# Kernel tuning notes

Hardware: AMD Instinct MI355X
Metric: run time of the kernel (lower is better)

The kernel has to match this reference:

```python
import jax, jax.numpy as jnp
import numpy as np
from functools import partial

N_NODES = 50000
N_EDGES = 600000
N_FEAT = 128
HID = [128, 64, 32, 16]
N_GRAPHS = 64
N_CLASSES = 10


def gcn_conv(x, W, b, src, dst, n_nodes):
    # PyG GCNConv: h = x @ W; propagate with symmetric norm over A + I; add bias.
    h = x @ W  # [N, out]
    ones = jnp.ones((src.shape[0],), dtype=x.dtype)
    deg = jax.ops.segment_sum(ones, dst, num_segments=n_nodes) + 1.0  # self-loop
    dinv = jax.lax.rsqrt(deg)
    coef = dinv[src] * dinv[dst]  # [E]
    agg = jax.ops.segment_sum(h[src] * coef[:, None], dst, num_segments=n_nodes)
    agg = agg + h * (dinv * dinv)[:, None]  # self-loop contribution
    return agg + b


def global_mean_pool(x, batch, n_graphs):
    s = jax.ops.segment_sum(x, batch, num_segments=n_graphs)
    cnt = jax.ops.segment_sum(jnp.ones((x.shape[0],), x.dtype), batch, num_segments=n_graphs)
    return s / jnp.maximum(cnt, 1.0)[:, None]


def setup_inputs() -> dict:
    key = jax.random.key(0)
    ks = jax.random.split(key, 16)
    x = jax.random.normal(ks[0], (N_NODES, N_FEAT), dtype=jnp.float32)
    edge_index = jax.random.randint(ks[1], (2, N_EDGES), 0, N_NODES, dtype=jnp.int64)
    batch = jnp.sort(jax.random.randint(ks[2], (N_NODES,), 0, N_GRAPHS, dtype=jnp.int64))

    def glorot(k, fan_in, fan_out):
        s = float(np.sqrt(6.0 / (fan_in + fan_out)))
        return jax.random.uniform(k, (fan_in, fan_out), jnp.float32, -s, s)

    dims = [N_FEAT] + HID
    params = {}
    for i in range(4):
        params[f"W{i+1}"] = glorot(ks[3 + i], dims[i], dims[i + 1])
        params[f"b{i+1}"] = jnp.zeros((dims[i + 1],), jnp.float32)
    params["Wlin"] = glorot(ks[7], HID[-1], N_CLASSES)
    params["blin"] = jnp.zeros((N_CLASSES,), jnp.float32)
    return {"x": x, "edge_index": edge_index, "batch": batch, **params}


def reference(x, edge_index, batch, W1, b1, W2, b2, W3, b3, W4, b4, Wlin, blin):
    src, dst = edge_index[0], edge_index[1]
    n = x.shape[0]
    h = jax.nn.relu(gcn_conv(x, W1, b1, src, dst, n))
    h = jax.nn.relu(gcn_conv(h, W2, b2, src, dst, n))
    h = jax.nn.relu(gcn_conv(h, W3, b3, src, dst, n))
    h = jax.nn.relu(gcn_conv(h, W4, b4, src, dst, n))
    g = global_mean_pool(h, batch, N_GRAPHS)  # [G, 16]
    return g @ Wlin + blin
```

## Files before the change

### kernel.cpp

```cpp
#include <hip/hip_runtime.h>
#include <hip/hip_bf16.h>


#define N_GRAPHS 64
#define N_CLASSES 10

typedef short bf8_t __attribute__((ext_vector_type(8)));
typedef float f4_t  __attribute__((ext_vector_type(4)));

__device__ __forceinline__ float b2f(unsigned int u) {
  return __uint_as_float(u << 16);
}
__device__ __forceinline__ unsigned short f2b(float f) {
  unsigned int x = __float_as_uint(f);
  x += 0x7fffu + ((x >> 16) & 1u);
  return (unsigned short)(x >> 16);
}

__device__ __forceinline__ void block_detect(const unsigned int* __restrict__ xraw,
    const unsigned int* __restrict__ eraw, int* f32, int* i64) {
  __shared__ int c_bf, c_nz;
  if (threadIdx.x == 0) { c_bf = 0; c_nz = 0; }
  __syncthreads();
  unsigned int d = xraw[threadIdx.x & 255];
  int e = (int)(((d & 0xffffu) >> 7) & 0xff);
  if (e >= 100 && e <= 140) atomicAdd(&c_bf, 1);
  if (eraw && threadIdx.x < 64 && eraw[2 * threadIdx.x + 1] != 0u) atomicAdd(&c_nz, 1);
  __syncthreads();
  *f32 = (c_bf < 150) ? 1 : 0;
  if (i64) *i64 = (c_nz == 0) ? 1 : 0;
}

struct WPtrs { const void* p[10]; };
static constexpr int WSEG[10] = {16384, 128, 8192, 64, 2048, 32, 512, 16, 160, 10};
static constexpr int WTOTAL   = 27546;
static constexpr int WOFF[10] = {0, 16384, 16512, 24704, 24768, 26816, 26848, 27360, 27376, 27536};

__global__ __launch_bounds__(256) void cvt_we_kernel(
    const unsigned int* __restrict__ xraw, WPtrs wp, unsigned short* __restrict__ wc,
    const int* __restrict__ braw, int* __restrict__ b32,
    const int* __restrict__ eraw, int* __restrict__ deg,
    int BW, int BB, int n, int E) {
  int f32, i64;
  block_detect(xraw, (const unsigned int*)eraw, &f32, &i64);
  const int bid = blockIdx.x;
  if (bid < BW) {
    int i = bid * 256 + threadIdx.x;
    if (i >= WTOTAL) return;
    int off = i, s = 0;
    #pragma unroll
    for (int t = 0; t < 10; ++t) {
      if (s == 0 && off >= WSEG[t]) { off -= WSEG[t]; } else if (s == 0) { s = t + 1; }
    }
    s -= 1;
    int soff = off;
    if ((s & 1) == 0 && s <= 6) {
      int KB, FOUT;
      if (s == 0)      { KB = 4; FOUT = 128; }
      else if (s == 2) { KB = 4; FOUT = 64; }
      else if (s == 4) { KB = 2; FOUT = 32; }
      else             { KB = 1; FOUT = 16; }
      int j = off & 7, l = (off >> 3) & 63, f = off >> 9;
      int ct = f / KB, kb = f - ct * KB;
      int k = kb * 32 + ((l >> 4) << 3) + j;
      int nn = ct * 16 + (l & 15);
      soff = k * FOUT + nn;
    }
    const void* p = wp.p[s];
    wc[WOFF[s] + off] = f32 ? f2b(((const float*)p)[soff])
                            : ((const unsigned short*)p)[soff];
  } else if (bid < BW + BB) {
    int i = (bid - BW) * 256 + threadIdx.x;
    if (i < n) b32[i] = i64 ? braw[2 * i] : braw[i];
  } else {
    int e = (bid - BW - BB) * 256 + threadIdx.x;
    if (e >= E) return;
    int d = i64 ? eraw[2 * (E + e)] : eraw[E + e];
    atomicAdd(&deg[d], 1);
  }
}

__global__ __launch_bounds__(256) void scan_kernel(const int* __restrict__ deg,
    int* __restrict__ row_ptr, int* __restrict__ cursor, float* __restrict__ dinv,
    unsigned long long* __restrict__ desc, int n) {
  __shared__ int ws[4];
  __shared__ int s_total;
  __shared__ unsigned int s_prev;
  const int b = blockIdx.x, tid = threadIdx.x, lane = tid & 63, wv = tid >> 6;
  const int i = b * 256 + tid;
  int v = (i < n) ? deg[i] : 0;
  int x = v;
  #pragma unroll
  for (int off = 1; off < 64; off <<= 1) {
    int y = __shfl_up(x, off, 64);
    if (lane >= off) x += y;
  }
  if (lane == 63) ws[wv] = x;
  __syncthreads();
  int wbase = 0;
  for (int w = 0; w < wv; ++w) wbase += ws[w];
  int incl = x + wbase;
  if (tid == 0) {
    int tot = ws[0] + ws[1] + ws[2] + ws[3];
    s_total = tot;
    unsigned long long st = (b == 0) ? (2ULL << 62) : (1ULL << 62);
    atomicExch(&desc[b], st | (unsigned long long)(unsigned int)tot);
    if (b == 0) s_prev = 0u;
  }
  __syncthreads();
  if (b > 0 && wv == 0) {
    unsigned int running = 0;
    int j = b - 1;
    while (true) {
      int idx = j - lane;
      unsigned long long d;
      if (idx >= 0) {
        do { d = atomicAdd(&desc[idx], 0ULL); } while ((d >> 62) == 0ULL);
      } else {
        d = (2ULL << 62);
      }
      unsigned long long ball = __ballot((d >> 62) == 2ULL);
      int fp = ball ? (__ffsll((unsigned long long)ball) - 1) : 64;
      unsigned int contrib = (lane <= fp) ? (unsigned int)(d & 0xffffffffULL) : 0u;
      #pragma unroll
      for (int o = 32; o; o >>= 1) contrib += __shfl_xor(contrib, o, 64);
      running += contrib;
      if (fp < 64) break;
      j -= 64;
    }
    if (lane == 0) {
      atomicExch(&desc[b], (2ULL << 62) |
                 (unsigned long long)(unsigned int)(running + (unsigned int)s_total));
      s_prev = running;
    }
  }
  __syncthreads();
  int tot = (int)s_prev + incl;
  if (i < n) {
    row_ptr[i + 1] = tot;
    cursor[i] = tot - v;
    dinv[i] = rsqrtf((float)v + 1.0f);
  }
  if (i == 0) row_ptr[0] = 0;
}

__global__ __launch_bounds__(256) void fill_gemm1_kernel(
    const int* __restrict__ eraw, const unsigned int* __restrict__ xraw,
    int* __restrict__ cursor, const float* __restrict__ dinv,
    uint2* __restrict__ csr,
    const unsigned short* __restrict__ Wf, unsigned short* __restrict__ H,
    int BE, int n, int E) {
  int f32, i64;
  block_detect(xraw, (const unsigned int*)eraw, &f32, &i64);
  if (blockIdx.x < BE) {
    int e = blockIdx.x * 256 + threadIdx.x;
    if (e < E) {
      int s, d;
      if (i64) { s = eraw[2 * e]; d = eraw[2 * (E + e)]; }
      else     { s = eraw[e];     d = eraw[E + e]; }
      int pos = atomicAdd(&cursor[d], 1);
      uint2 v;
      v.x = (unsigned int)s;
      v.y = __float_as_uint(dinv[s] * dinv[d]);
      csr[pos] = v;
    }
    return;
  }
  const int b2 = blockIdx.x - BE;
  const int l = threadIdx.x & 63;
  const int r16 = l & 15, quad = l >> 4;
  const int m0 = (b2 * 4 + (threadIdx.x >> 6)) * 32;
  if (m0 >= n) return;
  bf8_t afrag[2][4];
  #pragma unroll
  for (int mt = 0; mt < 2; ++mt) {
    int node = m0 + mt * 16 + r16;
    int nc = node < n ? node : n - 1;
    if (f32) {
      const float* xp = (const float*)xraw + (size_t)nc * 128 + quad * 8;
      #pragma unroll
      for (int kb = 0; kb < 4; ++kb) {
        const float4* p4 = (const float4*)(xp + kb * 32);
        float4 u0 = p4[0], u1 = p4[1];
        bf8_t a;
        a[0] = (short)f2b(u0.x); a[1] = (short)f2b(u0.y);
        a[2] = (short)f2b(u0.z); a[3] = (short)f2b(u0.w);
        a[4] = (short)f2b(u1.x); a[5] = (short)f2b(u1.y);
        a[6] = (short)f2b(u1.z); a[7] = (short)f2b(u1.w);
        afrag[mt][kb] = a;
      }
    } else {
      const unsigned short* xp = (const unsigned short*)xraw + (size_t)nc * 128 + quad * 8;
      #pragma unroll
      for (int kb = 0; kb < 4; ++kb)
        afrag[mt][kb] = *(const bf8_t*)(xp + kb * 32);
    }
  }
  #pragma unroll
  for (int ct = 0; ct < 8; ++ct) {
    bf8_t bfrag[4];
    #pragma unroll
    for (int kb = 0; kb < 4; ++kb)
      bfrag[kb] = *(const bf8_t*)(Wf + ((ct * 4 + kb) * 64 + l) * 8);
    #pragma unroll
    for (int mt = 0; mt < 2; ++mt) {
      f4_t acc = {0.f, 0.f, 0.f, 0.f};
      #pragma unroll
      for (int kb = 0; kb < 4; ++kb)
        acc = __builtin_amdgcn_mfma_f32_16x16x32_bf16(afrag[mt][kb], bfrag[kb], acc, 0, 0, 0);
      #pragma unroll
      for (int r = 0; r < 4; ++r) {
        int node = m0 + mt * 16 + quad * 4 + r;
        if (node < n)
          H[(size_t)node * 128 + ct * 16 + r16] = f2b(acc[r]);
      }
    }
  }
}

template<int DW> struct UVec { unsigned int d[DW]; };
template<int DW>
__device__ __forceinline__ UVec<DW> uload(const unsigned int* p) {
  UVec<DW> r;
  if constexpr (DW == 4) { uint4 v = *(const uint4*)p; r.d[0]=v.x; r.d[1]=v.y; r.d[2]=v.z; r.d[3]=v.w; }
  else if constexpr (DW == 2) { uint2 v = *(const uint2*)p; r.d[0]=v.x; r.d[1]=v.y; }
  else { r.d[0] = *p; }
  return r;
}
template<int DW>
__device__ __forceinline__ void ustore(unsigned int* p, const UVec<DW>& v) {
  if constexpr (DW == 4) { *(uint4*)p = make_uint4(v.d[0], v.d[1], v.d[2], v.d[3]); }
  else if constexpr (DW == 2) { *(uint2*)p = make_uint2(v.d[0], v.d[1]); }
  else { *p = v.d[0]; }
}

template<int FIN, int FOUT, int LPG>
__global__ __launch_bounds__(256) void aggemm_kernel(
    const unsigned short* __restrict__ Hin,
    const int* __restrict__ row_ptr, const uint2* __restrict__ csr,
    const float* __restrict__ dinv, const unsigned short* __restrict__ bias,
    const unsigned short* __restrict__ Wf, unsigned short* __restrict__ Hout, int n) {
  constexpr int DW  = FIN / LPG / 2;
  constexpr int NPB = 256 / LPG;
  constexpr int LD  = FIN + 8;
  constexpr int KB  = FIN / 32;
  constexpr int CT  = FOUT / 16;
  constexpr int MT  = NPB / 16;
  __shared__ unsigned short T[NPB * LD];
  const int r = threadIdx.x / LPG, l = threadIdx.x % LPG;
  const int node0 = blockIdx.x * NPB;
  const int g = node0 + r;
  const unsigned int* H2 = (const unsigned int*)Hin;
  UVec<DW> o;
  #pragma unroll
  for (int d = 0; d < DW; ++d) o.d[d] = 0u;
  if (g < n) {
    float di = dinv[g];
    float c0 = di * di;
    float a[2 * DW];
    UVec<DW> hv = uload<DW>(H2 + (size_t)g * (FIN / 2) + l * DW);
    #pragma unroll
    for (int d = 0; d < DW; ++d) {
      a[2*d]   = b2f(hv.d[d] & 0xffffu) * c0;
      a[2*d+1] = b2f(hv.d[d] >> 16) * c0;
    }
    const int e0 = row_ptr[g], e1 = row_ptr[g + 1];
    for (int base = e0; base < e1; base += LPG) {
      int cnt = e1 - base < LPG ? e1 - base : LPG;
      uint2 my = csr[(base + l < e1) ? (base + l) : (e1 - 1)];
      for (int j = 0; j < cnt; ++j) {
        int s = __shfl((int)my.x, j, LPG);
        float c = __uint_as_float(__shfl((int)my.y, j, LPG));
        UVec<DW> v = uload<DW>(H2 + (size_t)s * (FIN / 2) + l * DW);
        #pragma unroll
        for (int d = 0; d < DW; ++d) {
          a[2*d]   = fmaf(b2f(v.d[d] & 0xffffu), c, a[2*d]);
          a[2*d+1] = fmaf(b2f(v.d[d] >> 16), c, a[2*d+1]);
        }
      }
    }
    UVec<DW> bb = uload<DW>((const unsigned int*)bias + l * DW);
    #pragma unroll
    for (int d = 0; d < DW; ++d) {
      float lo = fmaxf(a[2*d]   + b2f(bb.d[d] & 0xffffu), 0.f);
      float hi = fmaxf(a[2*d+1] + b2f(bb.d[d] >> 16), 0.f);
      o.d[d] = (unsigned int)f2b(lo) | ((unsigned int)f2b(hi) << 16);
    }
  }
  ustore<DW>((unsigned int*)&T[r * LD + l * DW * 2], o);
  __syncthreads();
  const int w = threadIdx.x >> 6;
  if (w < MT * CT && node0 < n) {
    const int mt = w / CT, ct = w % CT;
    const int ll = threadIdx.x & 63;
    const int r16 = ll & 15, quad = ll >> 4;
    bf8_t afrag[KB], bfrag[KB];
    #pragma unroll
    for (int kb = 0; kb < KB; ++kb) {
      afrag[kb] = *(const bf8_t*)(&T[(mt * 16 + r16) * LD + quad * 8 + kb * 32]);
      bfrag[kb] = *(const bf8_t*)(Wf + ((ct * KB + kb) * 64 + ll) * 8);
    }
    f4_t acc = {0.f, 0.f, 0.f, 0.f};
    #pragma unroll
    for (int kb = 0; kb < KB; ++kb)
      acc = __builtin_amdgcn_mfma_f32_16x16x32_bf16(afrag[kb], bfrag[kb], acc, 0, 0, 0);
    #pragma unroll
    for (int rr = 0; rr < 4; ++rr) {
      int node = node0 + mt * 16 + quad * 4 + rr;
      if (node < n)
        Hout[(size_t)node * FOUT + ct * 16 + r16] = f2b(acc[rr]);
    }
  }
}

__global__ __launch_bounds__(256) void agg_pool_kernel(
    const unsigned short* __restrict__ Hin,
    const int* __restrict__ row_ptr, const uint2* __restrict__ csr,
    const float* __restrict__ dinv, const unsigned short* __restrict__ bias,
    const int* __restrict__ batch, float* __restrict__ pooled,
    float* __restrict__ cnt, int n) {
  __shared__ float acc[N_GRAPHS * 16];
  __shared__ float ccnt[N_GRAPHS];
  for (int i = threadIdx.x; i < N_GRAPHS * 16; i += 256) acc[i] = 0.f;
  if (threadIdx.x < N_GRAPHS) ccnt[threadIdx.x] = 0.f;
  __syncthreads();
  const int r = threadIdx.x >> 3, l = threadIdx.x & 7;
  const int g = blockIdx.x * 32 + r;
  if (g < n) {
    const unsigned int* H2 = (const unsigned int*)Hin;
    float di = dinv[g];
    float c0 = di * di;
    unsigned int hv = H2[(size_t)g * 8 + l];
    float a0 = b2f(hv & 0xffffu) * c0;
    float a1 = b2f(hv >> 16) * c0;
    const int e0 = row_ptr[g], e1 = row_ptr[g + 1];
    for (int base = e0; base < e1; base += 8) {
      int cnt2 = e1 - base < 8 ? e1 - base : 8;
      uint2 my = csr[(base + l < e1) ? (base + l) : (e1 - 1)];
      for (int j = 0; j < cnt2; ++j) {
        int s = __shfl((int)my.x, j, 8);
        float c = __uint_as_float(__shfl((int)my.y, j, 8));
        unsigned int v = H2[(size_t)s * 8 + l];
        a0 = fmaf(b2f(v & 0xffffu), c, a0);
        a1 = fmaf(b2f(v >> 16), c, a1);
      }
    }
    unsigned int bb = ((const unsigned int*)bias)[l];
    a0 = fmaxf(a0 + b2f(bb & 0xffffu), 0.f);
    a1 = fmaxf(a1 + b2f(bb >> 16), 0.f);
    int gb = batch[g];
    atomicAdd(&acc[gb * 16 + l * 2 + 0], a0);
    atomicAdd(&acc[gb * 16 + l * 2 + 1], a1);
    if (l == 0) atomicAdd(&ccnt[gb], 1.f);
  }
  __syncthreads();
  for (int i = threadIdx.x; i < N_GRAPHS * 16; i += 256)
    if (acc[i] != 0.f) atomicAdd(&pooled[i], acc[i]);
  if (threadIdx.x < N_GRAPHS && ccnt[threadIdx.x] != 0.f)
    atomicAdd(&cnt[threadIdx.x], ccnt[threadIdx.x]);
}

__global__ __launch_bounds__(256) void final_kernel(const float* __restrict__ pooled,
    const float* __restrict__ cnt, const unsigned short* __restrict__ wc,
    void* __restrict__ out, const unsigned int* __restrict__ xraw) {
  int f32;
  block_detect(xraw, nullptr, &f32, nullptr);
  int id = blockIdx.x * 256 + threadIdx.x;
  if (id >= N_GRAPHS * N_CLASSES) return;
  const unsigned short* Wlin = wc + WOFF[8];
  const unsigned short* blin = wc + WOFF[9];
  int g = id / N_CLASSES, c = id - g * N_CLASSES;
  float inv = 1.0f / fmaxf(cnt[g], 1.0f);
  float a = b2f(blin[c]);
  #pragma unroll
  for (int f = 0; f < 16; ++f)
    a = fmaf(pooled[g * 16 + f] * inv, b2f(Wlin[f * N_CLASSES + c]), a);
  if (f32) ((float*)out)[id] = a;
  else     ((unsigned short*)out)[id] = f2b(a);
}

extern "C" void kernel_launch(void* const* d_in, const int* in_sizes, int n_in,
                              void* d_out, int out_size, void* d_ws, size_t ws_size,
                              hipStream_t stream) {
  const unsigned int* xraw = (const unsigned int*)d_in[0];
  const int* eraw          = (const int*)d_in[1];
  const int* braw          = (const int*)d_in[2];

  const int N = in_sizes[2];
  const int E = in_sizes[1] / 2;
  const int nb = (N + 255) / 256;

  char* p = (char*)d_ws;
  auto alloc = [&](size_t bytes) -> void* {
    void* r = (void*)p;
    p += (bytes + 255) & ~(size_t)255;
    return r;
  };
  const size_t off_desc = ((size_t)N * 4 + 255) & ~(size_t)255;
  const size_t off_pool = (off_desc + (size_t)nb * 8 + 255) & ~(size_t)255;
  const size_t ztotal   = off_pool + (N_GRAPHS * 16 + N_GRAPHS) * 4;
  char* zbase = (char*)alloc(ztotal);
  int*   deg    = (int*)zbase;
  unsigned long long* desc = (unsigned long long*)(zbase + off_desc);
  float* pooled = (float*)(zbase + off_pool);
  float* cntf   = pooled + N_GRAPHS * 16;

  int*   row_ptr  = (int*)  alloc((size_t)(N + 1) * 4);
  int*   cursor   = (int*)  alloc((size_t)N * 4);
  float* dinv     = (float*)alloc((size_t)N * 4);
  int*   batch32  = (int*)  alloc((size_t)N * 4);
  uint2* csr      = (uint2*)alloc((size_t)E * 8);
  unsigned short* wcan  = (unsigned short*)alloc((size_t)WTOTAL * 2);
  unsigned short* hbufA = (unsigned short*)alloc((size_t)N * 128 * 2);
  unsigned short* hbufB = (unsigned short*)alloc((size_t)N * 128 * 2);

  hipMemsetAsync(zbase, 0, ztotal, stream);

  WPtrs wp;
  for (int i = 0; i < 10; ++i) wp.p[i] = d_in[3 + i];

  const int BW = (WTOTAL + 255) / 256;
  const int BB = nb;
  const int BE = (E + 255) / 256;
  cvt_we_kernel<<<BW + BB + BE, 256, 0, stream>>>(xraw, wp, wcan, braw, batch32,
      eraw, deg, BW, BB, N, E);

  scan_kernel<<<nb, 256, 0, stream>>>(deg, row_ptr, cursor, dinv, desc, N);

  const unsigned short* W1 = wcan + WOFF[0];
  const unsigned short* b1 = wcan + WOFF[1];
  const unsigned short* W2 = wcan + WOFF[2];
  const unsigned short* b2 = wcan + WOFF[3];
  const unsigned short* W3 = wcan + WOFF[4];
  const unsigned short* b3 = wcan + WOFF[5];
  const unsigned short* W4 = wcan + WOFF[6];
  const unsigned short* b4 = wcan + WOFF[7];

  const int G1 = (N + 127) / 128;
  fill_gemm1_kernel<<<BE + G1, 256, 0, stream>>>(eraw, xraw, cursor, dinv, csr,
      W1, hbufA, BE, N, E);

  aggemm_kernel<128, 64, 16><<<(N + 15) / 16, 256, 0, stream>>>(
      hbufA, row_ptr, csr, dinv, b1, W2, hbufB, N);
  aggemm_kernel<64, 32, 8><<<(N + 31) / 32, 256, 0, stream>>>(
      hbufB, row_ptr, csr, dinv, b2, W3, hbufA, N);
  aggemm_kernel<32, 16, 8><<<(N + 31) / 32, 256, 0, stream>>>(
      hbufA, row_ptr, csr, dinv, b3, W4, hbufB, N);
  agg_pool_kernel<<<(N + 31) / 32, 256, 0, stream>>>(hbufB, row_ptr, csr, dinv, b4,
      batch32, pooled, cntf, N);

  final_kernel<<<(N_GRAPHS * N_CLASSES + 255) / 256, 256, 0, stream>>>(pooled, cntf, wcan, d_out, xraw);
}
```

Before: 240.2 us.

## Fold symmetric norm into GEMM outputs and shard degree/cursor atomics eightfold

Each GEMM now scales its output rows by dinv[src], and each aggregation scales the summed neighbour rows by dinv[dst] at the end. This removes the per-edge coefficient, so the CSR holds only 4-byte source indices instead of 8-byte pairs and the inner loop is a plain add. Separately, the degree counts and fill cursors are split into 8 sub-arrays chosen by block index to cut atomic contention. The scan runs over 8N entries, and its shuffle reduction rebuilds the full degree. The cost is a larger scan and an extra bf16 rounding of the pre-scaled features.

```diff
diff --git a/kernel.cpp b/kernel.cpp
--- a/kernel.cpp
+++ b/kernel.cpp
@@ -39,7 +39,7 @@
 __global__ __launch_bounds__(256) void cvt_we_kernel(
     const unsigned int* __restrict__ xraw, WPtrs wp, unsigned short* __restrict__ wc,
     const int* __restrict__ braw, int* __restrict__ b32,
-    const int* __restrict__ eraw, int* __restrict__ deg,
+    const int* __restrict__ eraw, int* __restrict__ degs,
     int BW, int BB, int n, int E) {
   int f32, i64;
   block_detect(xraw, (const unsigned int*)eraw, &f32, &i64);
@@ -76,11 +76,11 @@
     int e = (bid - BW - BB) * 256 + threadIdx.x;
     if (e >= E) return;
     int d = i64 ? eraw[2 * (E + e)] : eraw[E + e];
-    atomicAdd(&deg[d], 1);
-  }
-}
-
-__global__ __launch_bounds__(256) void scan_kernel(const int* __restrict__ deg,
+    atomicAdd(&degs[(bid & 7) * n + d], 1);
+  }
+}
+
+__global__ __launch_bounds__(256) void scan_kernel(const int* __restrict__ degs,
     int* __restrict__ row_ptr, int* __restrict__ cursor, float* __restrict__ dinv,
     unsigned long long* __restrict__ desc, int n) {
   __shared__ int ws[4];
@@ -88,7 +88,8 @@
   __shared__ unsigned int s_prev;
   const int b = blockIdx.x, tid = threadIdx.x, lane = tid & 63, wv = tid >> 6;
   const int i = b * 256 + tid;
-  int v = (i < n) ? deg[i] : 0;
+  const int d = i >> 3, s = i & 7;
+  int v = (d < n) ? degs[s * n + d] : 0;
   int x = v;
   #pragma unroll
   for (int off = 1; off < 64; off <<= 1) {
@@ -113,15 +114,15 @@
     int j = b - 1;
     while (true) {
       int idx = j - lane;
-      unsigned long long d;
+      unsigned long long dsc;
       if (idx >= 0) {
-        do { d = atomicAdd(&desc[idx], 0ULL); } while ((d >> 62) == 0ULL);
+        do { dsc = atomicAdd(&desc[idx], 0ULL); } while ((dsc >> 62) == 0ULL);
       } else {
-        d = (2ULL << 62);
+        dsc = (2ULL << 62);
       }
-      unsigned long long ball = __ballot((d >> 62) == 2ULL);
+      unsigned long long ball = __ballot((dsc >> 62) == 2ULL);
       int fp = ball ? (__ffsll((unsigned long long)ball) - 1) : 64;
-      unsigned int contrib = (lane <= fp) ? (unsigned int)(d & 0xffffffffULL) : 0u;
+      unsigned int contrib = (lane <= fp) ? (unsigned int)(dsc & 0xffffffffULL) : 0u;
       #pragma unroll
       for (int o = 32; o; o >>= 1) contrib += __shfl_xor(contrib, o, 64);
       running += contrib;
@@ -136,10 +137,16 @@
   }
   __syncthreads();
   int tot = (int)s_prev + incl;
-  if (i < n) {
-    row_ptr[i + 1] = tot;
-    cursor[i] = tot - v;
-    dinv[i] = rsqrtf((float)v + 1.0f);
+  int rs = v;
+  rs += __shfl_xor(rs, 1, 64);
+  rs += __shfl_xor(rs, 2, 64);
+  rs += __shfl_xor(rs, 4, 64);
+  if (d < n) {
+    cursor[s * n + d] = tot - v;
+    if (s == 7) {
+      row_ptr[d + 1] = tot;
+      dinv[d] = rsqrtf((float)rs + 1.0f);
+    }
   }
   if (i == 0) row_ptr[0] = 0;
 }
@@ -147,7 +154,7 @@
 __global__ __launch_bounds__(256) void fill_gemm1_kernel(
     const int* __restrict__ eraw, const unsigned int* __restrict__ xraw,
     int* __restrict__ cursor, const float* __restrict__ dinv,
-    uint2* __restrict__ csr,
+    int* __restrict__ csr_src,
     const unsigned short* __restrict__ Wf, unsigned short* __restrict__ H,
     int BE, int n, int E) {
   int f32, i64;
@@ -158,11 +165,8 @@
       int s, d;
       if (i64) { s = eraw[2 * e]; d = eraw[2 * (E + e)]; }
       else     { s = eraw[e];     d = eraw[E + e]; }
-      int pos = atomicAdd(&cursor[d], 1);
-      uint2 v;
-      v.x = (unsigned int)s;
-      v.y = __float_as_uint(dinv[s] * dinv[d]);
-      csr[pos] = v;
+      int pos = atomicAdd(&cursor[(blockIdx.x & 7) * n + d], 1);
+      csr_src[pos] = s;
     }
     return;
   }
@@ -172,10 +176,16 @@
   const int m0 = (b2 * 4 + (threadIdx.x >> 6)) * 32;
   if (m0 >= n) return;
   bf8_t afrag[2][4];
+  float dv[2][4];
   #pragma unroll
   for (int mt = 0; mt < 2; ++mt) {
     int node = m0 + mt * 16 + r16;
     int nc = node < n ? node : n - 1;
+    #pragma unroll
+    for (int r = 0; r < 4; ++r) {
+      int nd = m0 + mt * 16 + quad * 4 + r;
+      dv[mt][r] = dinv[nd < n ? nd : n - 1];
+    }
     if (f32) {
       const float* xp = (const float*)xraw + (size_t)nc * 128 + quad * 8;
       #pragma unroll
@@ -212,7 +222,7 @@
       for (int r = 0; r < 4; ++r) {
         int node = m0 + mt * 16 + quad * 4 + r;
         if (node < n)
-          H[(size_t)node * 128 + ct * 16 + r16] = f2b(acc[r]);
+          H[(size_t)node * 128 + ct * 16 + r16] = f2b(acc[r] * dv[mt][r]);
       }
     }
   }
@@ -237,7 +247,7 @@
 template<int FIN, int FOUT, int LPG>
 __global__ __launch_bounds__(256) void aggemm_kernel(
     const unsigned short* __restrict__ Hin,
-    const int* __restrict__ row_ptr, const uint2* __restrict__ csr,
+    const int* __restrict__ row_ptr, const int* __restrict__ csr_src,
     const float* __restrict__ dinv, const unsigned short* __restrict__ bias,
     const unsigned short* __restrict__ Wf, unsigned short* __restrict__ Hout, int n) {
   constexpr int DW  = FIN / LPG / 2;
@@ -255,35 +265,33 @@
   #pragma unroll
   for (int d = 0; d < DW; ++d) o.d[d] = 0u;
   if (g < n) {
-    float di = dinv[g];
-    float c0 = di * di;
     float a[2 * DW];
     UVec<DW> hv = uload<DW>(H2 + (size_t)g * (FIN / 2) + l * DW);
     #pragma unroll
     for (int d = 0; d < DW; ++d) {
-      a[2*d]   = b2f(hv.d[d] & 0xffffu) * c0;
-      a[2*d+1] = b2f(hv.d[d] >> 16) * c0;
+      a[2*d]   = b2f(hv.d[d] & 0xffffu);
+      a[2*d+1] = b2f(hv.d[d] >> 16);
     }
     const int e0 = row_ptr[g], e1 = row_ptr[g + 1];
     for (int base = e0; base < e1; base += LPG) {
       int cnt = e1 - base < LPG ? e1 - base : LPG;
-      uint2 my = csr[(base + l < e1) ? (base + l) : (e1 - 1)];
+      int my = csr_src[(base + l < e1) ? (base + l) : (e1 - 1)];
       for (int j = 0; j < cnt; ++j) {
-        int s = __shfl((int)my.x, j, LPG);
-        float c = __uint_as_float(__shfl((int)my.y, j, LPG));
+        int s = __shfl(my, j, LPG);
         UVec<DW> v = uload<DW>(H2 + (size_t)s * (FIN / 2) + l * DW);
         #pragma unroll
         for (int d = 0; d < DW; ++d) {
-          a[2*d]   = fmaf(b2f(v.d[d] & 0xffffu), c, a[2*d]);
-          a[2*d+1] = fmaf(b2f(v.d[d] >> 16), c, a[2*d+1]);
+          a[2*d]   += b2f(v.d[d] & 0xffffu);
+          a[2*d+1] += b2f(v.d[d] >> 16);
         }
       }
     }
+    float di = dinv[g];
     UVec<DW> bb = uload<DW>((const unsigned int*)bias + l * DW);
     #pragma unroll
     for (int d = 0; d < DW; ++d) {
-      float lo = fmaxf(a[2*d]   + b2f(bb.d[d] & 0xffffu), 0.f);
-      float hi = fmaxf(a[2*d+1] + b2f(bb.d[d] >> 16), 0.f);
+      float lo = fmaxf(fmaf(a[2*d],   di, b2f(bb.d[d] & 0xffffu)), 0.f);
+      float hi = fmaxf(fmaf(a[2*d+1], di, b2f(bb.d[d] >> 16)), 0.f);
       o.d[d] = (unsigned int)f2b(lo) | ((unsigned int)f2b(hi) << 16);
     }
   }
@@ -294,6 +302,12 @@
     const int mt = w / CT, ct = w % CT;
     const int ll = threadIdx.x & 63;
     const int r16 = ll & 15, quad = ll >> 4;
+    float dvv[4];
+    #pragma unroll
+    for (int rr = 0; rr < 4; ++rr) {
+      int nd = node0 + mt * 16 + quad * 4 + rr;
+      dvv[rr] = dinv[nd < n ? nd : n - 1];
+    }
     bf8_t afrag[KB], bfrag[KB];
     #pragma unroll
     for (int kb = 0; kb < KB; ++kb) {
@@ -308,14 +322,14 @@
     for (int rr = 0; rr < 4; ++rr) {
       int node = node0 + mt * 16 + quad * 4 + rr;
       if (node < n)
-        Hout[(size_t)node * FOUT + ct * 16 + r16] = f2b(acc[rr]);
+        Hout[(size_t)node * FOUT + ct * 16 + r16] = f2b(acc[rr] * dvv[rr]);
     }
   }
 }
 
 __global__ __launch_bounds__(256) void agg_pool_kernel(
     const unsigned short* __restrict__ Hin,
-    const int* __restrict__ row_ptr, const uint2* __restrict__ csr,
+    const int* __restrict__ row_ptr, const int* __restrict__ csr_src,
     const float* __restrict__ dinv, const unsigned short* __restrict__ bias,
     const int* __restrict__ batch, float* __restrict__ pooled,
     float* __restrict__ cnt, int n) {
@@ -328,26 +342,24 @@
   const int g = blockIdx.x * 32 + r;
   if (g < n) {
     const unsigned int* H2 = (const unsigned int*)Hin;
-    float di = dinv[g];
-    float c0 = di * di;
     unsigned int hv = H2[(size_t)g * 8 + l];
-    float a0 = b2f(hv & 0xffffu) * c0;
-    float a1 = b2f(hv >> 16) * c0;
+    float a0 = b2f(hv & 0xffffu);
+    float a1 = b2f(hv >> 16);
     const int e0 = row_ptr[g], e1 = row_ptr[g + 1];
     for (int base = e0; base < e1; base += 8) {
       int cnt2 = e1 - base < 8 ? e1 - base : 8;
-      uint2 my = csr[(base + l < e1) ? (base + l) : (e1 - 1)];
+      int my = csr_src[(base + l < e1) ? (base + l) : (e1 - 1)];
       for (int j = 0; j < cnt2; ++j) {
-        int s = __shfl((int)my.x, j, 8);
-        float c = __uint_as_float(__shfl((int)my.y, j, 8));
+        int s = __shfl(my, j, 8);
         unsigned int v = H2[(size_t)s * 8 + l];
-        a0 = fmaf(b2f(v & 0xffffu), c, a0);
-        a1 = fmaf(b2f(v >> 16), c, a1);
+        a0 += b2f(v & 0xffffu);
+        a1 += b2f(v >> 16);
       }
     }
+    float di = dinv[g];
     unsigned int bb = ((const unsigned int*)bias)[l];
-    a0 = fmaxf(a0 + b2f(bb & 0xffffu), 0.f);
-    a1 = fmaxf(a1 + b2f(bb >> 16), 0.f);
+    a0 = fmaxf(fmaf(a0, di, b2f(bb & 0xffffu)), 0.f);
+    a1 = fmaxf(fmaf(a1, di, b2f(bb >> 16)), 0.f);
     int gb = batch[g];
     atomicAdd(&acc[gb * 16 + l * 2 + 0], a0);
     atomicAdd(&acc[gb * 16 + l * 2 + 1], a1);
@@ -388,7 +400,7 @@
 
   const int N = in_sizes[2];
   const int E = in_sizes[1] / 2;
-  const int nb = (N + 255) / 256;
+  const int nb2 = (8 * N + 255) / 256;
 
   char* p = (char*)d_ws;
   auto alloc = [&](size_t bytes) -> void* {
@@ -396,20 +408,20 @@
     p += (bytes + 255) & ~(size_t)255;
     return r;
   };
-  const size_t off_desc = ((size_t)N * 4 + 255) & ~(size_t)255;
-  const size_t off_pool = (off_desc + (size_t)nb * 8 + 255) & ~(size_t)255;
+  const size_t off_desc = ((size_t)8 * N * 4 + 255) & ~(size_t)255;
+  const size_t off_pool = (off_desc + (size_t)nb2 * 8 + 255) & ~(size_t)255;
   const size_t ztotal   = off_pool + (N_GRAPHS * 16 + N_GRAPHS) * 4;
   char* zbase = (char*)alloc(ztotal);
-  int*   deg    = (int*)zbase;
+  int*   degs   = (int*)zbase;
   unsigned long long* desc = (unsigned long long*)(zbase + off_desc);
   float* pooled = (float*)(zbase + off_pool);
   float* cntf   = pooled + N_GRAPHS * 16;
 
   int*   row_ptr  = (int*)  alloc((size_t)(N + 1) * 4);
-  int*   cursor   = (int*)  alloc((size_t)N * 4);
+  int*   cursor   = (int*)  alloc((size_t)8 * N * 4);
   float* dinv     = (float*)alloc((size_t)N * 4);
   int*   batch32  = (int*)  alloc((size_t)N * 4);
-  uint2* csr      = (uint2*)alloc((size_t)E * 8);
+  int*   csr_src  = (int*)  alloc((size_t)E * 4);
   unsigned short* wcan  = (unsigned short*)alloc((size_t)WTOTAL * 2);
   unsigned short* hbufA = (unsigned short*)alloc((size_t)N * 128 * 2);
   unsigned short* hbufB = (unsigned short*)alloc((size_t)N * 128 * 2);
@@ -420,12 +432,12 @@
   for (int i = 0; i < 10; ++i) wp.p[i] = d_in[3 + i];
 
   const int BW = (WTOTAL + 255) / 256;
-  const int BB = nb;
+  const int BB = (N + 255) / 256;
   const int BE = (E + 255) / 256;
   cvt_we_kernel<<<BW + BB + BE, 256, 0, stream>>>(xraw, wp, wcan, braw, batch32,
-      eraw, deg, BW, BB, N, E);
-
-  scan_kernel<<<nb, 256, 0, stream>>>(deg, row_ptr, cursor, dinv, desc, N);
+      eraw, degs, BW, BB, N, E);
+
+  scan_kernel<<<nb2, 256, 0, stream>>>(degs, row_ptr, cursor, dinv, desc, N);
 
   const unsigned short* W1 = wcan + WOFF[0];
   const unsigned short* b1 = wcan + WOFF[1];
@@ -437,16 +449,16 @@
   const unsigned short* b4 = wcan + WOFF[7];
 
   const int G1 = (N + 127) / 128;
-  fill_gemm1_kernel<<<BE + G1, 256, 0, stream>>>(eraw, xraw, cursor, dinv, csr,
+  fill_gemm1_kernel<<<BE + G1, 256, 0, stream>>>(eraw, xraw, cursor, dinv, csr_src,
       W1, hbufA, BE, N, E);
 
   aggemm_kernel<128, 64, 16><<<(N + 15) / 16, 256, 0, stream>>>(
-      hbufA, row_ptr, csr, dinv, b1, W2, hbufB, N);
+      hbufA, row_ptr, csr_src, dinv, b1, W2, hbufB, N);
   aggemm_kernel<64, 32, 8><<<(N + 31) / 32, 256, 0, stream>>>(
-      hbufB, row_ptr, csr, dinv, b2, W3, hbufA, N);
+      hbufB, row_ptr, csr_src, dinv, b2, W3, hbufA, N);
   aggemm_kernel<32, 16, 8><<<(N + 31) / 32, 256, 0, stream>>>(
-      hbufA, row_ptr, csr, dinv, b3, W4, hbufB, N);
-  agg_pool_kernel<<<(N + 31) / 32, 256, 0, stream>>>(hbufB, row_ptr, csr, dinv, b4,
+      hbufA, row_ptr, csr_src, dinv, b3, W4, hbufB, N);
+  agg_pool_kernel<<<(N + 31) / 32, 256, 0, stream>>>(hbufB, row_ptr, csr_src, dinv, b4,
       batch32, pooled, cntf, N);
 
   final_kernel<<<(N_GRAPHS * N_CLASSES + 255) / 256, 256, 0, stream>>>(pooled, cntf, wcan, d_out, xraw);
```

Result: slower. 252.1 us (+4.9%).
